# Optimization experiments

Hardware: AMD Instinct MI355X
Metric: run time of the kernel (lower is better)

Reference implementation:

```python
import jax, jax.numpy as jnp
import numpy as np
from jax import lax

N_J = 53
N_NAMES = 18
C_IN, C_OUT, K = 32, 32, 3
B, T = 16, 2048
# joint -> unique-name id (first-occurrence order of RELATED_NODES values)
NAME_IDS = np.array([0,1,2,3,4,1,2,3,4,5,6,7,8,9,10,11,12,13,14,15,16,14,15,16,14,15,16,14,15,16,14,15,16,10,11,12,13,14,15,16,14,15,16,14,15,16,14,15,16,14,15,16,17])
# adjacency: each joint attends to [self, parent] (uniform degree 2)
ADJ = np.array([[i, max(i - 1, 0)] for i in range(N_J)])


def setup_inputs() -> dict:
    key = jax.random.key(0)
    ks = jax.random.split(key, 5)
    return {
        "x": jax.random.normal(ks[0], (B, T, N_J, C_IN), jnp.float32),
        "lin_w": jax.random.normal(ks[1], (N_NAMES, 2 * C_IN, C_OUT), jnp.float32) / np.sqrt(2 * C_IN).astype(np.float32),
        "lin_b": jax.random.normal(ks[2], (N_NAMES, C_OUT), jnp.float32) * 0.01,
        "conv_w": jax.random.normal(ks[3], (N_NAMES, C_OUT, C_OUT, K), jnp.float32) / np.sqrt(C_OUT * K).astype(np.float32),
        "conv_b": jax.random.normal(ks[4], (N_NAMES, C_OUT), jnp.float32) * 0.01,
    }


def reference(x, lin_w, lin_b, conv_w, conv_b):
    Bb, Tt = x.shape[0], x.shape[1]
    # per-joint gather of [self, parent] neighbors: [B,T,J,2,Cin]
    gath = x[:, :, ADJ, :]
    feat = gath.reshape(Bb, Tt, N_J, 2 * C_IN)
    # shared-by-name Linear weights, gathered per joint
    Wj = lin_w[NAME_IDS]  # [J, 2Cin, Cout]
    bj = lin_b[NAME_IDS]  # [J, Cout]
    h = jax.nn.relu(jnp.einsum('btjf,jfo->btjo', feat, Wj) + bj)  # [B,T,J,Cout]
    # reflect-pad time axis (torch Conv1d padding_mode='reflect', padding=1)
    hp = jnp.pad(h, ((0, 0), (1, 1), (0, 0), (0, 0)), mode='reflect')
    # grouped 1D conv: one group per joint with its name's kernel
    hc = hp.transpose(0, 2, 3, 1).reshape(Bb, N_J * C_OUT, Tt + 2)  # [B, J*Cout, T+2]
    kw = conv_w[NAME_IDS].reshape(N_J * C_OUT, C_OUT, K)            # [J*Cout, Cout, K]
    y = lax.conv_general_dilated(hc, kw, (1,), 'VALID',
                                 dimension_numbers=('NCH', 'OIH', 'NCH'),
                                 feature_group_count=N_J)           # [B, J*Cout, T]
    y = y.reshape(Bb, N_J, C_OUT, Tt) + conv_b[NAME_IDS][None, :, :, None]
    return y.transpose(0, 3, 1, 2)  # [B, T, J, Cout]
```

## Files before the change

kernel.cpp:

```cpp
#include <hip/hip_runtime.h>
#include <hip/hip_bf16.h>
#include <cstddef>
#include <cstdint>

typedef __attribute__((ext_vector_type(8))) short short8_t;
typedef __attribute__((ext_vector_type(4))) float f32x4;
typedef __attribute__((ext_vector_type(2))) float f32x2;
typedef unsigned short ushort4a __attribute__((ext_vector_type(4)));

#define WAVE_FENCE()                                        \
  do {                                                      \
    asm volatile("s_waitcnt lgkmcnt(0)" ::: "memory");      \
    __builtin_amdgcn_sched_barrier(0);                      \
  } while (0)
#define VM_FENCE()                                          \
  do {                                                      \
    asm volatile("s_waitcnt vmcnt(0)" ::: "memory");        \
    __builtin_amdgcn_sched_barrier(0);                      \
  } while (0)

namespace {
constexpr int T = 2048;
constexpr int NB = 16;
constexpr int NJ = 53;
constexpr int NN = 18;
constexpr int TTILE = 256;
constexpr int NTILES = T / TTILE;
constexpr int MT_LIN = 17;
constexpr int MT_CNV = 16;
constexpr int HROWS = TTILE + 2;
constexpr int HSTR = 36;
constexpr int SSTR = 38;
constexpr int NBLK = NB * NJ * NTILES;
constexpr int XSPAN = NBLK / 8;
}

__constant__ int c_name_ids[NJ] = {
    0,1,2,3,4,1,2,3,4,5,6,7,8,9,10,11,12,13,14,15,16,14,15,16,14,15,16,
    14,15,16,14,15,16,10,11,12,13,14,15,16,14,15,16,14,15,16,14,15,16,
    14,15,16,17};

__device__ short8_t g_linfrag[NN][2][2][2][64];
__device__ short8_t g_convfrag[NN][3][2][2][64];

__device__ __forceinline__ unsigned short f2bf(float f) {
  return __builtin_bit_cast(unsigned short, __float2bfloat16(f));
}
__device__ __forceinline__ float bf2f(unsigned short u) {
  return __bfloat162float(__builtin_bit_cast(__hip_bfloat16, u));
}


__global__ __launch_bounds__(64)
void prep_weights(const float* __restrict__ lin_w,
                  const float* __restrict__ conv_w)
{
  const int n = blockIdx.x;
  const int l = threadIdx.x;
  const int r = l & 15;
  const int g = l >> 4;
#pragma unroll
  for (int ks = 0; ks < 2; ++ks)
#pragma unroll
    for (int nt = 0; nt < 2; ++nt) {
      short8_t hi8, lo8;
#pragma unroll
      for (int e = 0; e < 8; ++e) {
        const int kk = 4 * g + (e & 3) + 16 * (e >> 2);
        const float w = lin_w[((size_t)n * 64 + ks * 32 + kk) * 32 + r + 16 * nt];
        const unsigned short h = f2bf(w);
        hi8[e] = (short)h;
        lo8[e] = (short)f2bf(w - bf2f(h));
      }
      g_linfrag[n][ks][nt][0][l] = hi8;
      g_linfrag[n][ks][nt][1][l] = lo8;
    }
#pragma unroll
  for (int k = 0; k < 3; ++k)
#pragma unroll
    for (int nt = 0; nt < 2; ++nt) {
      short8_t hi8, lo8;
#pragma unroll
      for (int e = 0; e < 8; ++e) {
        const int i = 4 * g + (e & 3) + 16 * (e >> 2);
        const float w = conv_w[(((size_t)n * 32 + r + 16 * nt) * 32 + i) * 3 + k];
        const unsigned short h = f2bf(w);
        hi8[e] = (short)h;
        lo8[e] = (short)f2bf(w - bf2f(h));
      }
      g_convfrag[n][k][nt][0][l] = hi8;
      g_convfrag[n][k][nt][1][l] = lo8;
    }
}

__global__ __launch_bounds__(256, 4)
void fused_rcb_mfma(const float* __restrict__ x,
                    const float* __restrict__ lin_b,
                    const float* __restrict__ conv_b,
                    float* __restrict__ out)
{
  __shared__ __align__(16) unsigned short s_hi[HROWS * HSTR];
  __shared__ __align__(16) char s_feat[4][4096];

  const int raw = blockIdx.x;
  const int bid = (raw % 8) * XSPAN + (raw / 8);
  const int j    = bid % NJ;
  const int tile = (bid / NJ) % NTILES;
  const int b    = bid / (NJ * NTILES);
  const int nid  = c_name_ids[j];
  const int jp   = (j > 0) ? (j - 1) : 0;
  const int t0   = tile * TTILE;

  const int tid = threadIdx.x;
  const int wv = tid >> 6;
  const int l  = tid & 63;
  const int r  = l & 15;
  const int g  = l >> 4;

  char* featc = s_feat[wv];

  const float* xj_base = x + ((size_t)b * T * NJ + j) * 32;
  const float* xp_base = x + ((size_t)b * T * NJ + jp) * 32;

  short8_t blh[2][2], bll[2][2];
#pragma unroll
  for (int ks = 0; ks < 2; ++ks)
#pragma unroll
    for (int nt = 0; nt < 2; ++nt) {
      blh[ks][nt] = g_linfrag[nid][ks][nt][0][l];
      bll[ks][nt] = g_linfrag[nid][ks][nt][1][l];
    }
  const float lb0 = lin_b[nid * 32 + r];
  const float lb1 = lin_b[nid * 32 + r + 16];

  auto issue_feat = [&](int mt) {
#pragma unroll
    for (int j2 = 0; j2 < 2; ++j2) {
      const float* jb = j2 ? xp_base : xj_base;
#pragma unroll
      for (int i = 0; i < 2; ++i) {
        const int row = i * 8 + (l >> 3);
        int t = t0 + mt * 16 + row - 1;
        if (t < 0) t = -t;
        if (t > T - 1) t = 2 * (T - 1) - t;
        const char* src = reinterpret_cast<const char*>(jb + (size_t)t * (NJ * 32))
                          + (((l & 7) * 16) ^ ((row & 7) << 4));
        __builtin_amdgcn_global_load_lds(
            (const __attribute__((address_space(1))) unsigned int*)src,
            (__attribute__((address_space(3))) unsigned int*)(&s_feat[wv][j2 * 2048 + i * 1024]),
            16, 0, 0);
      }
    }
  };

  issue_feat(wv);
  for (int mt = wv; mt < MT_LIN; mt += 4) {
    VM_FENCE();

    f32x4 a0[2], a1[2];
#pragma unroll
    for (int ks = 0; ks < 2; ++ks) {
      const char* fw = featc + ks * 2048 + r * 128;
      a0[ks] = *reinterpret_cast<const f32x4*>(fw + ((16 * g) ^ ((r & 7) << 4)));
      a1[ks] = *reinterpret_cast<const f32x4*>(fw + ((64 + 16 * g) ^ ((r & 7) << 4)));
    }
    WAVE_FENCE();
    if (mt + 4 < MT_LIN) issue_feat(mt + 4);

    short8_t ah[2];
#pragma unroll
    for (int ks = 0; ks < 2; ++ks) {
#pragma unroll
      for (int e = 0; e < 8; ++e) {
        const float f = (e < 4) ? a0[ks][e] : a1[ks][e - 4];
        ah[ks][e] = (short)(unsigned short)(__builtin_bit_cast(uint32_t, f) >> 16);
      }
    }

#pragma unroll
    for (int nt = 0; nt < 2; ++nt) {
      const float lb = nt ? lb1 : lb0;
      f32x4 acc = {lb, lb, lb, lb};
#pragma unroll
      for (int ks = 0; ks < 2; ++ks) {
        acc = __builtin_amdgcn_mfma_f32_16x16x32_bf16(ah[ks], blh[ks][nt], acc, 0, 0, 0);
        acc = __builtin_amdgcn_mfma_f32_16x16x32_bf16(ah[ks], bll[ks][nt], acc, 0, 0, 0);
      }
#pragma unroll
      for (int q = 0; q < 4; ++q) {
        const int hrow = mt * 16 + 4 * g + q;
        if (hrow < HROWS)
          s_hi[hrow * HSTR + r + 16 * nt] = f2bf(fmaxf(acc[q], 0.0f));
      }
    }
  }

  short8_t bch[3][2], bcl[3][2];
#pragma unroll
  for (int k = 0; k < 3; ++k)
#pragma unroll
    for (int nt = 0; nt < 2; ++nt) {
      bch[k][nt] = g_convfrag[nid][k][nt][0][l];
      bcl[k][nt] = g_convfrag[nid][k][nt][1][l];
    }
  const float cb0 = conv_b[nid * 32 + r];
  const float cb1 = conv_b[nid * 32 + r + 16];

  __syncthreads();

  float* st = reinterpret_cast<float*>(featc);

  for (int mt = wv; mt < MT_CNV; mt += 4) {
    const int m0 = mt * 16;
    short8_t ah[3];
#pragma unroll
    for (int k = 0; k < 3; ++k) {
      const int arow = m0 + r + k;
      const ushort4a u0 = *reinterpret_cast<const ushort4a*>(&s_hi[arow * HSTR + 4 * g]);
      const ushort4a u1 = *reinterpret_cast<const ushort4a*>(&s_hi[arow * HSTR + 16 + 4 * g]);
      short8_t hi8;
#pragma unroll
      for (int e = 0; e < 4; ++e) {
        hi8[e] = (short)u0[e];
        hi8[e + 4] = (short)u1[e];
      }
      ah[k] = hi8;
    }

    f32x4 accv[2];
#pragma unroll
    for (int nt = 0; nt < 2; ++nt) {
      const float cb = nt ? cb1 : cb0;
      f32x4 acc = {cb, cb, cb, cb};
#pragma unroll
      for (int k = 0; k < 3; ++k) {
        acc = __builtin_amdgcn_mfma_f32_16x16x32_bf16(ah[k], bch[k][nt], acc, 0, 0, 0);
        acc = __builtin_amdgcn_mfma_f32_16x16x32_bf16(ah[k], bcl[k][nt], acc, 0, 0, 0);
      }
      accv[nt] = acc;
    }

    WAVE_FENCE();
#pragma unroll
    for (int nt = 0; nt < 2; ++nt)
#pragma unroll
      for (int q = 0; q < 4; ++q)
        st[(4 * g + q) * SSTR + r + 16 * nt] = accv[nt][q];
    WAVE_FENCE();

#pragma unroll
    for (int h2 = 0; h2 < 2; ++h2) {
      const int row = h2 * 8 + (l >> 3);
      const float* rp = st + row * SSTR + (l & 7) * 4;
      const f32x2 rd0 = *reinterpret_cast<const f32x2*>(rp);
      const f32x2 rd1 = *reinterpret_cast<const f32x2*>(rp + 2);
      f32x4 rd;
      rd[0] = rd0[0]; rd[1] = rd0[1]; rd[2] = rd1[0]; rd[3] = rd1[1];
      const int t = t0 + m0 + row;
      __builtin_nontemporal_store(rd, reinterpret_cast<f32x4*>(
          out + ((size_t)(b * T + t) * NJ + j) * 32 + (l & 7) * 4));
    }
  }
}

extern "C" void kernel_launch(void* const* d_in, const int* in_sizes, int n_in,
                              void* d_out, int out_size, void* d_ws, size_t ws_size,
                              hipStream_t stream) {
  const float* x      = (const float*)d_in[0];
  const float* lin_w  = (const float*)d_in[1];
  const float* lin_b  = (const float*)d_in[2];
  const float* conv_w = (const float*)d_in[3];
  const float* conv_b = (const float*)d_in[4];
  float* out = (float*)d_out;

  prep_weights<<<dim3(NN), 64, 0, stream>>>(lin_w, conv_w);
  fused_rcb_mfma<<<dim3(NBLK), 256, 0, stream>>>(x, lin_b, conv_b, out);
}
```

Before: 77.05 us.

## Convert fused kernel to persistent blocks that each loop over one joint's tiles

Replaces the one-block-per-(batch,tile,joint) grid with 1024 persistent blocks. Each block is assigned a single joint and iterates over a strided subset of the 128 (batch,tile) items. Weight fragments and biases are loaded once per block, and the first feature loads of the next item are issued before the loop-end barrier. The aim is to cut launch and per-block setup overhead and reuse the weights, at the cost of uneven work per block (19 or 20 blocks per joint) and extra barriers inside the loop.

```diff
diff --git a/kernel.cpp b/kernel.cpp
--- a/kernel.cpp
+++ b/kernel.cpp
@@ -31,8 +31,8 @@
 constexpr int HROWS = TTILE + 2;
 constexpr int HSTR = 36;
 constexpr int SSTR = 38;
-constexpr int NBLK = NB * NJ * NTILES;
-constexpr int XSPAN = NBLK / 8;
+constexpr int NITEMS = NB * NTILES;
+constexpr int NPERS = 1024;
 }
 
 __constant__ int c_name_ids[NJ] = {
@@ -102,14 +102,16 @@
   __shared__ __align__(16) unsigned short s_hi[HROWS * HSTR];
   __shared__ __align__(16) char s_feat[4][4096];
 
-  const int raw = blockIdx.x;
-  const int bid = (raw % 8) * XSPAN + (raw / 8);
-  const int j    = bid % NJ;
-  const int tile = (bid / NJ) % NTILES;
-  const int b    = bid / (NJ * NTILES);
-  const int nid  = c_name_ids[j];
-  const int jp   = (j > 0) ? (j - 1) : 0;
-  const int t0   = tile * TTILE;
+  const int B = blockIdx.x;
+  const int jB    = (53 * B) >> 10;
+  const int lo    = (jB * 1024 + 52) / 53;
+  const int hi    = ((jB + 1) * 1024 + 52) / 53;
+  const int nB    = hi - lo;
+  const int local = B - lo;
+
+  const int j   = jB;
+  const int nid = c_name_ids[j];
+  const int jp  = (j > 0) ? (j - 1) : 0;
 
   const int tid = threadIdx.x;
   const int wv = tid >> 6;
@@ -119,28 +121,14 @@
 
   char* featc = s_feat[wv];
 
-  const float* xj_base = x + ((size_t)b * T * NJ + j) * 32;
-  const float* xp_base = x + ((size_t)b * T * NJ + jp) * 32;
-
-  short8_t blh[2][2], bll[2][2];
-#pragma unroll
-  for (int ks = 0; ks < 2; ++ks)
-#pragma unroll
-    for (int nt = 0; nt < 2; ++nt) {
-      blh[ks][nt] = g_linfrag[nid][ks][nt][0][l];
-      bll[ks][nt] = g_linfrag[nid][ks][nt][1][l];
-    }
-  const float lb0 = lin_b[nid * 32 + r];
-  const float lb1 = lin_b[nid * 32 + r + 16];
-
-  auto issue_feat = [&](int mt) {
+  auto issue_feat = [&](const float* xj_b, const float* xp_b, int t0_, int mt) {
 #pragma unroll
     for (int j2 = 0; j2 < 2; ++j2) {
-      const float* jb = j2 ? xp_base : xj_base;
+      const float* jb = j2 ? xp_b : xj_b;
 #pragma unroll
       for (int i = 0; i < 2; ++i) {
         const int row = i * 8 + (l >> 3);
-        int t = t0 + mt * 16 + row - 1;
+        int t = t0_ + mt * 16 + row - 1;
         if (t < 0) t = -t;
         if (t > T - 1) t = 2 * (T - 1) - t;
         const char* src = reinterpret_cast<const char*>(jb + (size_t)t * (NJ * 32))
@@ -153,48 +141,26 @@
     }
   };
 
-  issue_feat(wv);
-  for (int mt = wv; mt < MT_LIN; mt += 4) {
-    VM_FENCE();
-
-    f32x4 a0[2], a1[2];
-#pragma unroll
-    for (int ks = 0; ks < 2; ++ks) {
-      const char* fw = featc + ks * 2048 + r * 128;
-      a0[ks] = *reinterpret_cast<const f32x4*>(fw + ((16 * g) ^ ((r & 7) << 4)));
-      a1[ks] = *reinterpret_cast<const f32x4*>(fw + ((64 + 16 * g) ^ ((r & 7) << 4)));
-    }
-    WAVE_FENCE();
-    if (mt + 4 < MT_LIN) issue_feat(mt + 4);
-
-    short8_t ah[2];
-#pragma unroll
-    for (int ks = 0; ks < 2; ++ks) {
-#pragma unroll
-      for (int e = 0; e < 8; ++e) {
-        const float f = (e < 4) ? a0[ks][e] : a1[ks][e - 4];
-        ah[ks][e] = (short)(unsigned short)(__builtin_bit_cast(uint32_t, f) >> 16);
-      }
-    }
-
-#pragma unroll
-    for (int nt = 0; nt < 2; ++nt) {
-      const float lb = nt ? lb1 : lb0;
-      f32x4 acc = {lb, lb, lb, lb};
-#pragma unroll
-      for (int ks = 0; ks < 2; ++ks) {
-        acc = __builtin_amdgcn_mfma_f32_16x16x32_bf16(ah[ks], blh[ks][nt], acc, 0, 0, 0);
-        acc = __builtin_amdgcn_mfma_f32_16x16x32_bf16(ah[ks], bll[ks][nt], acc, 0, 0, 0);
-      }
-#pragma unroll
-      for (int q = 0; q < 4; ++q) {
-        const int hrow = mt * 16 + 4 * g + q;
-        if (hrow < HROWS)
-          s_hi[hrow * HSTR + r + 16 * nt] = f2bf(fmaxf(acc[q], 0.0f));
-      }
-    }
-  }
-
+  int b_cur, t0;
+  const float *xj_base, *xp_base;
+  auto set_bases = [&](int s) {
+    b_cur = s >> 3;
+    t0 = (s & 7) * TTILE;
+    xj_base = x + ((size_t)b_cur * T * NJ + j) * 32;
+    xp_base = x + ((size_t)b_cur * T * NJ + jp) * 32;
+  };
+
+  set_bases(local);
+  issue_feat(xj_base, xp_base, t0, wv);
+
+  short8_t blh[2][2], bll[2][2];
+#pragma unroll
+  for (int ks = 0; ks < 2; ++ks)
+#pragma unroll
+    for (int nt = 0; nt < 2; ++nt) {
+      blh[ks][nt] = g_linfrag[nid][ks][nt][0][l];
+      bll[ks][nt] = g_linfrag[nid][ks][nt][1][l];
+    }
   short8_t bch[3][2], bcl[3][2];
 #pragma unroll
   for (int k = 0; k < 3; ++k)
@@ -203,62 +169,117 @@
       bch[k][nt] = g_convfrag[nid][k][nt][0][l];
       bcl[k][nt] = g_convfrag[nid][k][nt][1][l];
     }
+  const float lb0 = lin_b[nid * 32 + r];
+  const float lb1 = lin_b[nid * 32 + r + 16];
   const float cb0 = conv_b[nid * 32 + r];
   const float cb1 = conv_b[nid * 32 + r + 16];
 
-  __syncthreads();
-
-  float* st = reinterpret_cast<float*>(featc);
-
-  for (int mt = wv; mt < MT_CNV; mt += 4) {
-    const int m0 = mt * 16;
-    short8_t ah[3];
-#pragma unroll
-    for (int k = 0; k < 3; ++k) {
-      const int arow = m0 + r + k;
-      const ushort4a u0 = *reinterpret_cast<const ushort4a*>(&s_hi[arow * HSTR + 4 * g]);
-      const ushort4a u1 = *reinterpret_cast<const ushort4a*>(&s_hi[arow * HSTR + 16 + 4 * g]);
-      short8_t hi8;
-#pragma unroll
-      for (int e = 0; e < 4; ++e) {
-        hi8[e] = (short)u0[e];
-        hi8[e + 4] = (short)u1[e];
-      }
-      ah[k] = hi8;
-    }
-
-    f32x4 accv[2];
-#pragma unroll
-    for (int nt = 0; nt < 2; ++nt) {
-      const float cb = nt ? cb1 : cb0;
-      f32x4 acc = {cb, cb, cb, cb};
+  for (int s = local; s < NITEMS; s += nB) {
+    const int  snx      = s + nB;
+    const bool has_next = snx < NITEMS;
+
+    for (int mt = wv; mt < MT_LIN; mt += 4) {
+      VM_FENCE();
+
+      f32x4 a0[2], a1[2];
+#pragma unroll
+      for (int ks = 0; ks < 2; ++ks) {
+        const char* fw = featc + ks * 2048 + r * 128;
+        a0[ks] = *reinterpret_cast<const f32x4*>(fw + ((16 * g) ^ ((r & 7) << 4)));
+        a1[ks] = *reinterpret_cast<const f32x4*>(fw + ((64 + 16 * g) ^ ((r & 7) << 4)));
+      }
+      WAVE_FENCE();
+      if (mt + 4 < MT_LIN) issue_feat(xj_base, xp_base, t0, mt + 4);
+
+      short8_t ah[2];
+#pragma unroll
+      for (int ks = 0; ks < 2; ++ks) {
+#pragma unroll
+        for (int e = 0; e < 8; ++e) {
+          const float f = (e < 4) ? a0[ks][e] : a1[ks][e - 4];
+          ah[ks][e] = (short)(unsigned short)(__builtin_bit_cast(uint32_t, f) >> 16);
+        }
+      }
+
+#pragma unroll
+      for (int nt = 0; nt < 2; ++nt) {
+        const float lb = nt ? lb1 : lb0;
+        f32x4 acc = {lb, lb, lb, lb};
+#pragma unroll
+        for (int ks = 0; ks < 2; ++ks) {
+          acc = __builtin_amdgcn_mfma_f32_16x16x32_bf16(ah[ks], blh[ks][nt], acc, 0, 0, 0);
+          acc = __builtin_amdgcn_mfma_f32_16x16x32_bf16(ah[ks], bll[ks][nt], acc, 0, 0, 0);
+        }
+#pragma unroll
+        for (int q = 0; q < 4; ++q) {
+          const int hrow = mt * 16 + 4 * g + q;
+          if (hrow < HROWS)
+            s_hi[hrow * HSTR + r + 16 * nt] = f2bf(fmaxf(acc[q], 0.0f));
+        }
+      }
+    }
+
+    WAVE_FENCE();
+    __builtin_amdgcn_s_barrier();
+
+    float* st = reinterpret_cast<float*>(featc);
+    for (int mt = wv; mt < MT_CNV; mt += 4) {
+      const int m0 = mt * 16;
+      short8_t ah[3];
 #pragma unroll
       for (int k = 0; k < 3; ++k) {
-        acc = __builtin_amdgcn_mfma_f32_16x16x32_bf16(ah[k], bch[k][nt], acc, 0, 0, 0);
-        acc = __builtin_amdgcn_mfma_f32_16x16x32_bf16(ah[k], bcl[k][nt], acc, 0, 0, 0);
-      }
-      accv[nt] = acc;
-    }
-
-    WAVE_FENCE();
-#pragma unroll
-    for (int nt = 0; nt < 2; ++nt)
-#pragma unroll
-      for (int q = 0; q < 4; ++q)
-        st[(4 * g + q) * SSTR + r + 16 * nt] = accv[nt][q];
-    WAVE_FENCE();
-
-#pragma unroll
-    for (int h2 = 0; h2 < 2; ++h2) {
-      const int row = h2 * 8 + (l >> 3);
-      const float* rp = st + row * SSTR + (l & 7) * 4;
-      const f32x2 rd0 = *reinterpret_cast<const f32x2*>(rp);
-      const f32x2 rd1 = *reinterpret_cast<const f32x2*>(rp + 2);
-      f32x4 rd;
-      rd[0] = rd0[0]; rd[1] = rd0[1]; rd[2] = rd1[0]; rd[3] = rd1[1];
-      const int t = t0 + m0 + row;
-      __builtin_nontemporal_store(rd, reinterpret_cast<f32x4*>(
-          out + ((size_t)(b * T + t) * NJ + j) * 32 + (l & 7) * 4));
+        const int arow = m0 + r + k;
+        const ushort4a u0 = *reinterpret_cast<const ushort4a*>(&s_hi[arow * HSTR + 4 * g]);
+        const ushort4a u1 = *reinterpret_cast<const ushort4a*>(&s_hi[arow * HSTR + 16 + 4 * g]);
+        short8_t hi8;
+#pragma unroll
+        for (int e = 0; e < 4; ++e) {
+          hi8[e] = (short)u0[e];
+          hi8[e + 4] = (short)u1[e];
+        }
+        ah[k] = hi8;
+      }
+
+      f32x4 accv[2];
+#pragma unroll
+      for (int nt = 0; nt < 2; ++nt) {
+        const float cb = nt ? cb1 : cb0;
+        f32x4 acc = {cb, cb, cb, cb};
+#pragma unroll
+        for (int k = 0; k < 3; ++k) {
+          acc = __builtin_amdgcn_mfma_f32_16x16x32_bf16(ah[k], bch[k][nt], acc, 0, 0, 0);
+          acc = __builtin_amdgcn_mfma_f32_16x16x32_bf16(ah[k], bcl[k][nt], acc, 0, 0, 0);
+        }
+        accv[nt] = acc;
+      }
+
+      WAVE_FENCE();
+#pragma unroll
+      for (int nt = 0; nt < 2; ++nt)
+#pragma unroll
+        for (int q = 0; q < 4; ++q)
+          st[(4 * g + q) * SSTR + r + 16 * nt] = accv[nt][q];
+      WAVE_FENCE();
+
+#pragma unroll
+      for (int h2 = 0; h2 < 2; ++h2) {
+        const int row = h2 * 8 + (l >> 3);
+        const float* rp = st + row * SSTR + (l & 7) * 4;
+        const f32x2 rd0 = *reinterpret_cast<const f32x2*>(rp);
+        const f32x2 rd1 = *reinterpret_cast<const f32x2*>(rp + 2);
+        f32x4 rd;
+        rd[0] = rd0[0]; rd[1] = rd0[1]; rd[2] = rd1[0]; rd[3] = rd1[1];
+        const int t = t0 + m0 + row;
+        __builtin_nontemporal_store(rd, reinterpret_cast<f32x4*>(
+            out + ((size_t)(b_cur * T + t) * NJ + j) * 32 + (l & 7) * 4));
+      }
+    }
+
+    if (has_next) {
+      set_bases(snx);
+      WAVE_FENCE();
+      issue_feat(xj_base, xp_base, t0, wv);
+      __builtin_amdgcn_s_barrier();
     }
   }
 }
@@ -274,5 +295,5 @@
   float* out = (float*)d_out;
 
   prep_weights<<<dim3(NN), 64, 0, stream>>>(lin_w, conv_w);
-  fused_rcb_mfma<<<dim3(NBLK), 256, 0, stream>>>(x, lin_b, conv_b, out);
-}
+  fused_rcb_mfma<<<dim3(NPERS), 256, 0, stream>>>(x, lin_b, conv_b, out);
+}
```

After: 141.7 us. 1.84x slower.

## Give each wave a private time slab with halo to drop block barrier

Applied to the files above, without the earlier changes.

Each wave now computes its own 64-row time slice plus a two-row halo of the linear+ReLU stage into a per-wave LDS region, so the conv stage only needs a wave-local fence instead of a block-wide __syncthreads. This removes inter-wave synchronization so waves can run the two stages independently. In exchange each wave recomputes halo rows (5 linear tiles per wave instead of about 4.25 on average) and LDS use grows by four private h buffers, which may reduce occupancy. The first feature load is also issued before the weight-fragment loads to overlap them.

```diff
diff --git a/kernel.cpp b/kernel.cpp
--- a/kernel.cpp
+++ b/kernel.cpp
@@ -26,9 +26,10 @@
 constexpr int NN = 18;
 constexpr int TTILE = 256;
 constexpr int NTILES = T / TTILE;
-constexpr int MT_LIN = 17;
-constexpr int MT_CNV = 16;
-constexpr int HROWS = TTILE + 2;
+constexpr int WROWS = 64;
+constexpr int LT_W = 5;
+constexpr int CT_W = 4;
+constexpr int HREG = WROWS + 2;
 constexpr int HSTR = 36;
 constexpr int SSTR = 38;
 constexpr int NBLK = NB * NJ * NTILES;
@@ -99,7 +100,7 @@
                     const float* __restrict__ conv_b,
                     float* __restrict__ out)
 {
-  __shared__ __align__(16) unsigned short s_hi[HROWS * HSTR];
+  __shared__ __align__(16) unsigned short s_hi[4][HREG * HSTR];
   __shared__ __align__(16) char s_feat[4][4096];
 
   const int raw = blockIdx.x;
@@ -118,43 +119,46 @@
   const int g  = l >> 4;
 
   char* featc = s_feat[wv];
+  unsigned short* hreg = s_hi[wv];
+  const int R0 = t0 + wv * WROWS;
 
   const float* xj_base = x + ((size_t)b * T * NJ + j) * 32;
   const float* xp_base = x + ((size_t)b * T * NJ + jp) * 32;
 
-  short8_t blh[2][2], bll[2][2];
-#pragma unroll
-  for (int ks = 0; ks < 2; ++ks)
-#pragma unroll
-    for (int nt = 0; nt < 2; ++nt) {
-      blh[ks][nt] = g_linfrag[nid][ks][nt][0][l];
-      bll[ks][nt] = g_linfrag[nid][ks][nt][1][l];
-    }
-  const float lb0 = lin_b[nid * 32 + r];
-  const float lb1 = lin_b[nid * 32 + r + 16];
-
-  auto issue_feat = [&](int mt) {
+  auto issue_feat = [&](int i) {
 #pragma unroll
     for (int j2 = 0; j2 < 2; ++j2) {
       const float* jb = j2 ? xp_base : xj_base;
 #pragma unroll
-      for (int i = 0; i < 2; ++i) {
-        const int row = i * 8 + (l >> 3);
-        int t = t0 + mt * 16 + row - 1;
+      for (int hg = 0; hg < 2; ++hg) {
+        const int row = hg * 8 + (l >> 3);
+        int t = R0 - 1 + i * 16 + row;
         if (t < 0) t = -t;
         if (t > T - 1) t = 2 * (T - 1) - t;
         const char* src = reinterpret_cast<const char*>(jb + (size_t)t * (NJ * 32))
                           + (((l & 7) * 16) ^ ((row & 7) << 4));
         __builtin_amdgcn_global_load_lds(
             (const __attribute__((address_space(1))) unsigned int*)src,
-            (__attribute__((address_space(3))) unsigned int*)(&s_feat[wv][j2 * 2048 + i * 1024]),
+            (__attribute__((address_space(3))) unsigned int*)(&s_feat[wv][j2 * 2048 + hg * 1024]),
             16, 0, 0);
       }
     }
   };
 
-  issue_feat(wv);
-  for (int mt = wv; mt < MT_LIN; mt += 4) {
+  issue_feat(0);
+
+  short8_t blh[2][2], bll[2][2];
+#pragma unroll
+  for (int ks = 0; ks < 2; ++ks)
+#pragma unroll
+    for (int nt = 0; nt < 2; ++nt) {
+      blh[ks][nt] = g_linfrag[nid][ks][nt][0][l];
+      bll[ks][nt] = g_linfrag[nid][ks][nt][1][l];
+    }
+  const float lb0 = lin_b[nid * 32 + r];
+  const float lb1 = lin_b[nid * 32 + r + 16];
+
+  for (int i = 0; i < LT_W; ++i) {
     VM_FENCE();
 
     f32x4 a0[2], a1[2];
@@ -165,7 +169,7 @@
       a1[ks] = *reinterpret_cast<const f32x4*>(fw + ((64 + 16 * g) ^ ((r & 7) << 4)));
     }
     WAVE_FENCE();
-    if (mt + 4 < MT_LIN) issue_feat(mt + 4);
+    if (i + 1 < LT_W) issue_feat(i + 1);
 
     short8_t ah[2];
 #pragma unroll
@@ -188,12 +192,14 @@
       }
 #pragma unroll
       for (int q = 0; q < 4; ++q) {
-        const int hrow = mt * 16 + 4 * g + q;
-        if (hrow < HROWS)
-          s_hi[hrow * HSTR + r + 16 * nt] = f2bf(fmaxf(acc[q], 0.0f));
+        const int hrow = i * 16 + 4 * g + q;
+        if (hrow < HREG)
+          hreg[hrow * HSTR + r + 16 * nt] = f2bf(fmaxf(acc[q], 0.0f));
       }
     }
   }
+
+  WAVE_FENCE();
 
   short8_t bch[3][2], bcl[3][2];
 #pragma unroll
@@ -206,18 +212,15 @@
   const float cb0 = conv_b[nid * 32 + r];
   const float cb1 = conv_b[nid * 32 + r + 16];
 
-  __syncthreads();
-
   float* st = reinterpret_cast<float*>(featc);
 
-  for (int mt = wv; mt < MT_CNV; mt += 4) {
-    const int m0 = mt * 16;
+  for (int ct = 0; ct < CT_W; ++ct) {
     short8_t ah[3];
 #pragma unroll
     for (int k = 0; k < 3; ++k) {
-      const int arow = m0 + r + k;
-      const ushort4a u0 = *reinterpret_cast<const ushort4a*>(&s_hi[arow * HSTR + 4 * g]);
-      const ushort4a u1 = *reinterpret_cast<const ushort4a*>(&s_hi[arow * HSTR + 16 + 4 * g]);
+      const int arow = ct * 16 + r + k;
+      const ushort4a u0 = *reinterpret_cast<const ushort4a*>(&hreg[arow * HSTR + 4 * g]);
+      const ushort4a u1 = *reinterpret_cast<const ushort4a*>(&hreg[arow * HSTR + 16 + 4 * g]);
       short8_t hi8;
 #pragma unroll
       for (int e = 0; e < 4; ++e) {
@@ -256,7 +259,7 @@
       const f32x2 rd1 = *reinterpret_cast<const f32x2*>(rp + 2);
       f32x4 rd;
       rd[0] = rd0[0]; rd[1] = rd0[1]; rd[2] = rd1[0]; rd[3] = rd1[1];
-      const int t = t0 + m0 + row;
+      const int t = R0 + ct * 16 + row;
       __builtin_nontemporal_store(rd, reinterpret_cast<f32x4*>(
           out + ((size_t)(b * T + t) * NJ + j) * 32 + (l & 7) * 4));
     }
```

After: 80.76 us. +4.8%, slower.
